# Optimization experiments

Hardware: AMD Instinct MI355X
Metric: run time of the kernel (lower is better)

Reference implementation:

```python
import jax, jax.numpy as jnp
import numpy as np

NEG_SLOPE = 0.2


def add_self_loops(edge_index, num_nodes):
    loop = jnp.arange(num_nodes, dtype=edge_index.dtype)
    return jnp.concatenate([edge_index, jnp.stack([loop, loop])], axis=1)


def gat_conv(x, edge_index, W, att_src, att_dst, bias, heads, out_ch, concat):
    # x: [N, F_in]; edge_index: [2, E]; W: [F_in, heads*out_ch]
    # att_src/att_dst: [heads, out_ch]; bias: [heads*out_ch] or [out_ch]
    N = x.shape[0]
    ei = add_self_loops(edge_index, N)
    src, dst = ei[0], ei[1]
    xw = (x @ W).reshape(N, heads, out_ch)          # [N, H, C]
    a_src = jnp.einsum('nhc,hc->nh', xw, att_src)    # [N, H]
    a_dst = jnp.einsum('nhc,hc->nh', xw, att_dst)    # [N, H]
    e = a_src[src] + a_dst[dst]                      # [E', H]
    e = jax.nn.leaky_relu(e, NEG_SLOPE)
    # segment softmax over edges grouped by destination node
    e_max = jax.ops.segment_max(e, dst, num_segments=N)  # [N, H]
    e_exp = jnp.exp(e - e_max[dst])
    denom = jax.ops.segment_sum(e_exp, dst, num_segments=N)  # [N, H]
    alpha = e_exp / denom[dst]                       # [E', H]
    msg = xw[src] * alpha[:, :, None]                # [E', H, C]
    out = jax.ops.segment_sum(msg, dst, num_segments=N)  # [N, H, C]
    if concat:
        out = out.reshape(N, heads * out_ch)
    else:
        out = out.mean(axis=1)
    return out + bias


def setup_inputs() -> dict:
    key = jax.random.key(0)
    ks = jax.random.split(key, 10)
    N, E = 100000, 1600000
    F_in, hid, heads, F_out = 128, 32, 4, 40
    s = 0.1
    x = jax.random.normal(ks[0], (N, F_in), dtype=jnp.float32)
    edge_index = jax.random.randint(ks[1], (2, E), 0, N, dtype=jnp.int64)
    W1 = jax.random.normal(ks[2], (F_in, heads * hid), dtype=jnp.float32) * s
    att_src1 = jax.random.normal(ks[3], (heads, hid), dtype=jnp.float32) * s
    att_dst1 = jax.random.normal(ks[4], (heads, hid), dtype=jnp.float32) * s
    b1 = jax.random.normal(ks[5], (heads * hid,), dtype=jnp.float32) * s
    W2 = jax.random.normal(ks[6], (heads * hid, F_out), dtype=jnp.float32) * s
    att_src2 = jax.random.normal(ks[7], (1, F_out), dtype=jnp.float32) * s
    att_dst2 = jax.random.normal(ks[8], (1, F_out), dtype=jnp.float32) * s
    b2 = jax.random.normal(ks[9], (F_out,), dtype=jnp.float32) * s
    return {"x": x, "edge_index": edge_index, "W1": W1, "att_src1": att_src1,
            "att_dst1": att_dst1, "b1": b1, "W2": W2, "att_src2": att_src2,
            "att_dst2": att_dst2, "b2": b2}


def reference(x, edge_index, W1, att_src1, att_dst1, b1, W2, att_src2, att_dst2, b2):
    h = gat_conv(x, edge_index, W1, att_src1, att_dst1, b1, heads=4, out_ch=32, concat=True)
    h = jax.nn.relu(h)
    out = gat_conv(h, edge_index, W2, att_src2, att_dst2, b2, heads=1, out_ch=40, concat=True)
    return out
```

## Files before the change

kernel.cpp:

```cpp
#include <hip/hip_runtime.h>
#include <hip/hip_bf16.h>

#define NEG_SLOPE 0.2f

typedef _Float16 f16;
typedef f16 f16x8 __attribute__((ext_vector_type(8)));
typedef float f32x4 __attribute__((ext_vector_type(4)));

__device__ __forceinline__ float lrelu(float v) { return v > 0.f ? v : NEG_SLOPE * v; }

__device__ __forceinline__ unsigned pack_h2(float a, float b) {
    union { f16 h[2]; unsigned u; } c;
    c.h[0] = (f16)a; c.h[1] = (f16)b;
    return c.u;
}
__device__ __forceinline__ float2 unpack_h2(unsigned u) {
    union { unsigned u; f16 h[2]; } c;
    c.u = u;
    return make_float2((float)c.h[0], (float)c.h[1]);
}

__global__ void k_detect(const int* __restrict__ ei32, int npairs, int* flag) {
    __shared__ int found;
    if (threadIdx.x == 0) found = 0;
    __syncthreads();
    for (int i = threadIdx.x; i < npairs; i += blockDim.x) {
        if (ei32[2 * i + 1] != 0) found = 1;
    }
    __syncthreads();
    if (threadIdx.x == 0) *flag = found ? 0 : 1;
}

__device__ __forceinline__ void load_edge(const void* ei, int f64, int e, int E, int& s, int& d) {
    if (f64) {
        const long long* p = (const long long*)ei;
        s = (int)p[e];
        d = (int)p[(long long)E + e];
    } else {
        const int* p = (const int*)ei;
        s = p[e];
        d = p[E + e];
    }
}

__global__ void k_degree(const void* __restrict__ ei, const int* __restrict__ flag,
                         int* __restrict__ deg, int* __restrict__ rank, int E) {
    int e = blockIdx.x * blockDim.x + threadIdx.x;
    if (e >= E) return;
    int s, d;
    load_edge(ei, *flag, e, E, s, d);
    rank[e] = atomicAdd(&deg[d], 1);
}

__global__ __launch_bounds__(1024) void k_scan_blk(const int* __restrict__ deg,
                                                   int* __restrict__ offsets,
                                                   int* __restrict__ blksum, int N) {
    __shared__ int wsums[16];
    const int t = threadIdx.x;
    const int lane = t & 63;
    const int wid = t >> 6;
    int idx = blockIdx.x * 4096 + t * 4;
    int v0 = (idx + 0 < N) ? deg[idx + 0] : 0;
    int v1 = (idx + 1 < N) ? deg[idx + 1] : 0;
    int v2 = (idx + 2 < N) ? deg[idx + 2] : 0;
    int v3 = (idx + 3 < N) ? deg[idx + 3] : 0;
    int s1 = v0 + v1, s2 = s1 + v2, s3 = s2 + v3;
    int inc = s3;
#pragma unroll
    for (int off = 1; off < 64; off <<= 1) {
        int y = __shfl_up(inc, off);
        if (lane >= off) inc += y;
    }
    if (lane == 63) wsums[wid] = inc;
    __syncthreads();
    if (wid == 0) {
        int v = (lane < 16) ? wsums[lane] : 0;
        int wi = v;
#pragma unroll
        for (int off = 1; off < 16; off <<= 1) {
            int y = __shfl_up(wi, off);
            if (lane >= off) wi += y;
        }
        if (lane < 16) wsums[lane] = wi - v;
        if (lane == 15) blksum[blockIdx.x] = wi;
    }
    __syncthreads();
    int excl = wsums[wid] + (inc - s3);
    if (idx + 0 < N) offsets[idx + 1] = excl + v0;
    if (idx + 1 < N) offsets[idx + 2] = excl + s1;
    if (idx + 2 < N) offsets[idx + 3] = excl + s2;
    if (idx + 3 < N) offsets[idx + 4] = excl + s3;
}

__global__ void k_scan_top(const int* __restrict__ blksum, int* __restrict__ blkoff, int G) {
    int l = threadIdx.x;
    int v = (l < G) ? blksum[l] : 0;
    int inc = v;
#pragma unroll
    for (int off = 1; off < 64; off <<= 1) {
        int y = __shfl_up(inc, off);
        if (l >= off) inc += y;
    }
    if (l < G) blkoff[l] = inc - v;
}

__global__ void k_scan_add(int* __restrict__ offsets, const int* __restrict__ blkoff, int N) {
    int n = blockIdx.x * blockDim.x + threadIdx.x;
    if (n >= N) return;
    offsets[n + 1] += blkoff[n >> 12];
    if (n == 0) offsets[0] = 0;
}

__global__ void k_scatter(const void* __restrict__ ei, const int* __restrict__ flag,
                          const int* __restrict__ offsets, const int* __restrict__ rank,
                          int* __restrict__ csr_src, int E) {
    int e = blockIdx.x * blockDim.x + threadIdx.x;
    if (e >= E) return;
    int s, d;
    load_edge(ei, *flag, e, E, s, d);
    csr_src[offsets[d] + rank[e]] = s;
}

__global__ void k_prep(const float* __restrict__ W1, const float* __restrict__ W2,
                       f16* __restrict__ W1t, f16* __restrict__ W2t) {
    int o = blockIdx.x * 256 + threadIdx.x;
    if (o < 128 * 128) {
        int n = o >> 7, k = o & 127;
        W1t[o] = (f16)W1[k * 128 + n];
    } else {
        int o2 = o - 128 * 128;
        if (o2 < 48 * 128) {
            int n = o2 >> 7, k = o2 & 127;
            W2t[o2] = (f16)(n < 40 ? W2[k * 40 + n] : 0.f);
        }
    }
}

__global__ __launch_bounds__(256) void k_gemm1(const float* __restrict__ X,
                                               const f16* __restrict__ W1t,
                                               f16* __restrict__ Af, int N) {
    __shared__ f16 sA[64 * 136];
    __shared__ f16 sB[128 * 136];
    const int t = threadIdx.x;
    const int row0 = blockIdx.x * 64;

    {
        int r = t >> 2, seg = t & 3;
        int row = row0 + r;
        if (row >= N) row = N - 1;
        const float4* xg = (const float4*)(X + (size_t)row * 128 + seg * 32);
        unsigned tmp[16];
#pragma unroll
        for (int j = 0; j < 8; j++) {
            float4 v = xg[j];
            tmp[2 * j]     = pack_h2(v.x, v.y);
            tmp[2 * j + 1] = pack_h2(v.z, v.w);
        }
        uint4* dst = (uint4*)&sA[r * 136 + seg * 32];
#pragma unroll
        for (int j = 0; j < 4; j++) dst[j] = ((uint4*)tmp)[j];
        int n = t >> 1, half = (t & 1) * 64;
        const uint4* src = (const uint4*)(W1t + n * 128 + half);
        uint4* dw = (uint4*)&sB[n * 136 + half];
#pragma unroll
        for (int j = 0; j < 8; j++) dw[j] = src[j];
    }
    __syncthreads();

    const int w = t >> 6, lane = t & 63, ln = lane & 15, q = lane >> 4;
    f32x4 acc[8];
#pragma unroll
    for (int c = 0; c < 8; c++) acc[c] = (f32x4){0.f, 0.f, 0.f, 0.f};

#pragma unroll
    for (int ks = 0; ks < 4; ks++) {
        f16x8 a = *(const f16x8*)&sA[(w * 16 + ln) * 136 + ks * 32 + q * 8];
#pragma unroll
        for (int c = 0; c < 8; c++) {
            f16x8 b = *(const f16x8*)&sB[(c * 16 + ln) * 136 + ks * 32 + q * 8];
            acc[c] = __builtin_amdgcn_mfma_f32_16x16x32_f16(a, b, acc[c], 0, 0, 0);
        }
    }

#pragma unroll
    for (int c = 0; c < 8; c++)
#pragma unroll
        for (int reg = 0; reg < 4; reg++) {
            int rg = row0 + w * 16 + q * 4 + reg;
            if (rg < N) Af[(size_t)rg * 128 + c * 16 + ln] = (f16)acc[c][reg];
        }
}

__global__ __launch_bounds__(256) void k_gemm2(const f16* __restrict__ Hf,
                                               const f16* __restrict__ W2t,
                                               f16* __restrict__ X2f, int N) {
    __shared__ f16 sA[64 * 136];
    __shared__ f16 sB[48 * 136];
    const int t = threadIdx.x;
    const int row0 = blockIdx.x * 64;
    {
        int r = t >> 2, seg = t & 3;
        int row = row0 + r;
        if (row >= N) row = N - 1;
        const uint4* hg = (const uint4*)(Hf + (size_t)row * 128 + seg * 32);
        uint4* dst = (uint4*)&sA[r * 136 + seg * 32];
#pragma unroll
        for (int j = 0; j < 4; j++) dst[j] = hg[j];
        const uint4* wsrc = (const uint4*)W2t;
#pragma unroll
        for (int u = t; u < 768; u += 256) {
            int o = u * 8;
            int n = o >> 7, ko = o & 127;
            *(uint4*)&sB[n * 136 + ko] = wsrc[u];
        }
    }
    __syncthreads();

    const int w = t >> 6, lane = t & 63, ln = lane & 15, q = lane >> 4;
    f32x4 acc[3];
#pragma unroll
    for (int c = 0; c < 3; c++) acc[c] = (f32x4){0.f, 0.f, 0.f, 0.f};

#pragma unroll
    for (int ks = 0; ks < 4; ks++) {
        f16x8 a = *(const f16x8*)&sA[(w * 16 + ln) * 136 + ks * 32 + q * 8];
#pragma unroll
        for (int c = 0; c < 3; c++) {
            f16x8 b = *(const f16x8*)&sB[(c * 16 + ln) * 136 + ks * 32 + q * 8];
            acc[c] = __builtin_amdgcn_mfma_f32_16x16x32_f16(a, b, acc[c], 0, 0, 0);
        }
    }

#pragma unroll
    for (int c = 0; c < 3; c++) {
        int col = c * 16 + ln;
        if (col < 40) {
#pragma unroll
            for (int reg = 0; reg < 4; reg++) {
                int rg = row0 + w * 16 + q * 4 + reg;
                if (rg < N) X2f[(size_t)rg * 40 + col] = (f16)acc[c][reg];
            }
        }
    }
}

__global__ void k_attn1(const f16* __restrict__ Af, const float* __restrict__ att_s,
                        const float* __restrict__ att_d, float* __restrict__ aS,
                        float* __restrict__ aD, int N) {
    int t = blockIdx.x * blockDim.x + threadIdx.x;
    if (t >= N * 4) return;
    int n = t >> 2, h = t & 3;
    const uint4* xr = (const uint4*)(Af + (size_t)n * 128 + h * 32);
    float ss = 0.f, sd = 0.f;
#pragma unroll
    for (int j = 0; j < 4; j++) {
        uint4 p = xr[j];
        float2 a0 = unpack_h2(p.x), a1 = unpack_h2(p.y), a2 = unpack_h2(p.z), a3 = unpack_h2(p.w);
        float xv[8] = {a0.x, a0.y, a1.x, a1.y, a2.x, a2.y, a3.x, a3.y};
        const float* as_ = att_s + h * 32 + j * 8;
        const float* ad_ = att_d + h * 32 + j * 8;
#pragma unroll
        for (int qq = 0; qq < 8; qq++) {
            ss += xv[qq] * as_[qq];
            sd += xv[qq] * ad_[qq];
        }
    }
    aS[t] = ss;
    aD[t] = sd;
}

__global__ void k_attn2(const f16* __restrict__ X2f, const float* __restrict__ att_s,
                        const float* __restrict__ att_d, float* __restrict__ aS,
                        float* __restrict__ aD, int N) {
    int n = blockIdx.x * blockDim.x + threadIdx.x;
    if (n >= N) return;
    const unsigned* xr = (const unsigned*)(X2f + (size_t)n * 40);
    float ss = 0.f, sd = 0.f;
#pragma unroll
    for (int j = 0; j < 20; j++) {
        float2 v = unpack_h2(xr[j]);
        ss += v.x * att_s[2 * j] + v.y * att_s[2 * j + 1];
        sd += v.x * att_d[2 * j] + v.y * att_d[2 * j + 1];
    }
    aS[n] = ss;
    aD[n] = sd;
}

__global__ __launch_bounds__(256) void k_alpha1(const int* __restrict__ offsets,
                                                const int* __restrict__ csr_src,
                                                const float* __restrict__ aS,
                                                const float* __restrict__ aD,
                                                float* __restrict__ alphaF,
                                                float* __restrict__ selfA, int N) {
    int n = blockIdx.x * 4 + (threadIdx.x >> 6);
    if (n >= N) return;
    int lane = threadIdx.x & 63;
    float4 aDn = *(const float4*)(aD + (size_t)n * 4);
    float4 aSn = *(const float4*)(aS + (size_t)n * 4);
    float r0 = 0.f, r1 = 0.f, r2 = 0.f, r3 = 0.f;
    int b = offsets[n], e = offsets[n + 1];
    for (int i = b + lane; i < e; i += 64) {
        int s = csr_src[i];
        float4 v = *(const float4*)(aS + (size_t)s * 4);
        r0 += __expf(lrelu(v.x + aDn.x));
        r1 += __expf(lrelu(v.y + aDn.y));
        r2 += __expf(lrelu(v.z + aDn.z));
        r3 += __expf(lrelu(v.w + aDn.w));
    }
#pragma unroll
    for (int m = 1; m < 64; m <<= 1) {
        r0 += __shfl_xor(r0, m);
        r1 += __shfl_xor(r1, m);
        r2 += __shfl_xor(r2, m);
        r3 += __shfl_xor(r3, m);
    }
    float w0 = __expf(lrelu(aSn.x + aDn.x));
    float w1 = __expf(lrelu(aSn.y + aDn.y));
    float w2 = __expf(lrelu(aSn.z + aDn.z));
    float w3 = __expf(lrelu(aSn.w + aDn.w));
    float i0 = 1.f / (r0 + w0), i1 = 1.f / (r1 + w1), i2 = 1.f / (r2 + w2), i3 = 1.f / (r3 + w3);
    if (lane == 0)
        *(float4*)(selfA + (size_t)n * 4) = make_float4(w0 * i0, w1 * i1, w2 * i2, w3 * i3);
    for (int i = b + lane; i < e; i += 64) {
        int s = csr_src[i];
        float4 v = *(const float4*)(aS + (size_t)s * 4);
        float4 al;
        al.x = __expf(lrelu(v.x + aDn.x)) * i0;
        al.y = __expf(lrelu(v.y + aDn.y)) * i1;
        al.z = __expf(lrelu(v.z + aDn.z)) * i2;
        al.w = __expf(lrelu(v.w + aDn.w)) * i3;
        *(float4*)(alphaF + (size_t)i * 4) = al;
    }
}

__global__ __launch_bounds__(256) void k_alpha2(const int* __restrict__ offsets,
                                                const int* __restrict__ csr_src,
                                                const float* __restrict__ aS,
                                                const float* __restrict__ aD,
                                                float* __restrict__ alpha,
                                                float* __restrict__ selfA, int N) {
    int n = blockIdx.x * 4 + (threadIdx.x >> 6);
    if (n >= N) return;
    int lane = threadIdx.x & 63;
    float aDn = aD[n];
    float r0 = 0.f;
    int b = offsets[n], e = offsets[n + 1];
    for (int i = b + lane; i < e; i += 64) {
        r0 += __expf(lrelu(aS[csr_src[i]] + aDn));
    }
#pragma unroll
    for (int m = 1; m < 64; m <<= 1) r0 += __shfl_xor(r0, m);
    float w0 = __expf(lrelu(aS[n] + aDn));
    float inv = 1.f / (r0 + w0);
    if (lane == 0) selfA[n] = w0 * inv;
    for (int i = b + lane; i < e; i += 64) {
        alpha[i] = __expf(lrelu(aS[csr_src[i]] + aDn)) * inv;
    }
}

__global__ __launch_bounds__(256) void k_msg1(const int* __restrict__ offsets,
                                              const int* __restrict__ csr_src,
                                              const float* __restrict__ alphaF,
                                              const float* __restrict__ selfA,
                                              const f16* __restrict__ Af,
                                              const float* __restrict__ b1,
                                              f16* __restrict__ Hf, int N) {
    int n = blockIdx.x * 4 + (threadIdx.x >> 6);
    if (n >= N) return;
    int lane = threadIdx.x & 63;
    int c0 = lane * 2;
    int h = lane >> 4;
    float sa = selfA[n * 4 + h];
    float2 pv = unpack_h2(*(const unsigned*)(Af + (size_t)n * 128 + c0));
    float acc0 = sa * pv.x, acc1 = sa * pv.y;
    int b = offsets[n], e = offsets[n + 1];
    int i = b;
    for (; i + 4 <= e; i += 4) {
        int s0 = csr_src[i], s1 = csr_src[i + 1], s2 = csr_src[i + 2], s3 = csr_src[i + 3];
        float a0 = alphaF[(size_t)i * 4 + h];
        float a1 = alphaF[(size_t)(i + 1) * 4 + h];
        float a2 = alphaF[(size_t)(i + 2) * 4 + h];
        float a3 = alphaF[(size_t)(i + 3) * 4 + h];
        unsigned r0 = *(const unsigned*)(Af + (size_t)s0 * 128 + c0);
        unsigned r1 = *(const unsigned*)(Af + (size_t)s1 * 128 + c0);
        unsigned r2 = *(const unsigned*)(Af + (size_t)s2 * 128 + c0);
        unsigned r3 = *(const unsigned*)(Af + (size_t)s3 * 128 + c0);
        float2 f0 = unpack_h2(r0), f1 = unpack_h2(r1), f2 = unpack_h2(r2), f3 = unpack_h2(r3);
        acc0 = fmaf(a0, f0.x, acc0); acc1 = fmaf(a0, f0.y, acc1);
        acc0 = fmaf(a1, f1.x, acc0); acc1 = fmaf(a1, f1.y, acc1);
        acc0 = fmaf(a2, f2.x, acc0); acc1 = fmaf(a2, f2.y, acc1);
        acc0 = fmaf(a3, f3.x, acc0); acc1 = fmaf(a3, f3.y, acc1);
    }
    for (; i < e; i++) {
        int s0 = csr_src[i];
        float a0 = alphaF[(size_t)i * 4 + h];
        float2 f0 = unpack_h2(*(const unsigned*)(Af + (size_t)s0 * 128 + c0));
        acc0 = fmaf(a0, f0.x, acc0); acc1 = fmaf(a0, f0.y, acc1);
    }
    float2 bb = *(const float2*)(b1 + c0);
    *(unsigned*)(Hf + (size_t)n * 128 + c0) =
        pack_h2(fmaxf(acc0 + bb.x, 0.f), fmaxf(acc1 + bb.y, 0.f));
}

__global__ __launch_bounds__(256) void k_msg2(const int* __restrict__ offsets,
                                              const int* __restrict__ csr_src,
                                              const float* __restrict__ alpha,
                                              const float* __restrict__ selfA,
                                              const f16* __restrict__ X2f,
                                              const float* __restrict__ b2,
                                              float* __restrict__ OUT, int N) {
    int wv = threadIdx.x >> 6, lane = threadIdx.x & 63;
    if (lane >= 60) return;
    int g = lane / 20;
    int li = lane - g * 20;
    int n = blockIdx.x * 12 + wv * 3 + g;
    if (n >= N) return;
    int c0 = li * 2;
    float sa = selfA[n];
    float2 pv = unpack_h2(*(const unsigned*)(X2f + (size_t)n * 40 + c0));
    float acc0 = sa * pv.x, acc1 = sa * pv.y;
    int b = offsets[n], e = offsets[n + 1];
    int i = b;
    for (; i + 4 <= e; i += 4) {
        int s0 = csr_src[i], s1 = csr_src[i + 1], s2 = csr_src[i + 2], s3 = csr_src[i + 3];
        float a0 = alpha[i], a1 = alpha[i + 1], a2 = alpha[i + 2], a3 = alpha[i + 3];
        float2 f0 = unpack_h2(*(const unsigned*)(X2f + (size_t)s0 * 40 + c0));
        float2 f1 = unpack_h2(*(const unsigned*)(X2f + (size_t)s1 * 40 + c0));
        float2 f2 = unpack_h2(*(const unsigned*)(X2f + (size_t)s2 * 40 + c0));
        float2 f3 = unpack_h2(*(const unsigned*)(X2f + (size_t)s3 * 40 + c0));
        acc0 += a0 * f0.x + a1 * f1.x + a2 * f2.x + a3 * f3.x;
        acc1 += a0 * f0.y + a1 * f1.y + a2 * f2.y + a3 * f3.y;
    }
    for (; i < e; i++) {
        int s0 = csr_src[i];
        float a0 = alpha[i];
        float2 f0 = unpack_h2(*(const unsigned*)(X2f + (size_t)s0 * 40 + c0));
        acc0 += a0 * f0.x;
        acc1 += a0 * f0.y;
    }
    float2 bb = *(const float2*)(b2 + c0);
    *(float2*)(OUT + (size_t)n * 40 + c0) = make_float2(acc0 + bb.x, acc1 + bb.y);
}

extern "C" void kernel_launch(void* const* d_in, const int* in_sizes, int n_in,
                              void* d_out, int out_size, void* d_ws, size_t ws_size,
                              hipStream_t stream) {
    const float* x   = (const float*)d_in[0];
    const void*  ei  = d_in[1];
    const float* W1  = (const float*)d_in[2];
    const float* as1 = (const float*)d_in[3];
    const float* ad1 = (const float*)d_in[4];
    const float* b1  = (const float*)d_in[5];
    const float* W2  = (const float*)d_in[6];
    const float* as2 = (const float*)d_in[7];
    const float* ad2 = (const float*)d_in[8];
    const float* b2  = (const float*)d_in[9];
    float* out = (float*)d_out;

    const int N = in_sizes[0] / 128;
    const int E = in_sizes[1] / 2;

    char* w = (char*)d_ws;
    auto alloc = [&](size_t bytes) {
        char* p = w;
        w += (bytes + 15) & ~(size_t)15;
        return p;
    };
    int* flag      = (int*)alloc(16);
    int* offsets   = (int*)alloc((size_t)(N + 1) * 4);
    int* deg       = (int*)alloc((size_t)N * 4);
    int* rank      = (int*)alloc((size_t)E * 4);
    int* csr_src   = (int*)alloc((size_t)E * 4);
    int* blksum    = (int*)alloc(64 * 4);
    int* blkoff    = (int*)alloc(64 * 4);
    float* aS1     = (float*)alloc((size_t)N * 4 * 4);
    float* aD1     = (float*)alloc((size_t)N * 4 * 4);
    float* aS2     = (float*)alloc((size_t)N * 4);
    float* aD2     = (float*)alloc((size_t)N * 4);
    float* alphaF  = (float*)alloc((size_t)E * 4 * 4);
    float* alpha2F = (float*)alloc((size_t)E * 4);
    float* selfA1  = (float*)alloc((size_t)N * 4 * 4);
    float* selfA2  = (float*)alloc((size_t)N * 4);
    f16* W1t       = (f16*)alloc(128 * 128 * 2);
    f16* W2t       = (f16*)alloc(48 * 128 * 2);
    f16* Af        = (f16*)alloc((size_t)N * 128 * 2);
    f16* X2f       = (f16*)alloc((size_t)N * 40 * 2);
    f16* Hf        = (f16*)alloc((size_t)N * 128 * 2);

    k_detect<<<1, 256, 0, stream>>>((const int*)ei, 1024, flag);
    k_prep<<<88, 256, 0, stream>>>(W1, W2, W1t, W2t);

    hipMemsetAsync(deg, 0, (size_t)N * 4, stream);
    k_degree<<<(E + 255) / 256, 256, 0, stream>>>(ei, flag, deg, rank, E);
    const int G = (N + 4095) / 4096;
    k_scan_blk<<<G, 1024, 0, stream>>>(deg, offsets, blksum, N);
    k_scan_top<<<1, 64, 0, stream>>>(blksum, blkoff, G);
    k_scan_add<<<(N + 255) / 256, 256, 0, stream>>>(offsets, blkoff, N);
    k_scatter<<<(E + 255) / 256, 256, 0, stream>>>(ei, flag, offsets, rank, csr_src, E);

    const int gb = (N + 63) / 64;
    k_gemm1<<<gb, 256, 0, stream>>>(x, W1t, Af, N);
    k_attn1<<<(N * 4 + 255) / 256, 256, 0, stream>>>(Af, as1, ad1, aS1, aD1, N);
    k_alpha1<<<(N + 3) / 4, 256, 0, stream>>>(offsets, csr_src, aS1, aD1, alphaF, selfA1, N);
    k_msg1<<<(N + 3) / 4, 256, 0, stream>>>(offsets, csr_src, alphaF, selfA1, Af, b1, Hf, N);

    k_gemm2<<<gb, 256, 0, stream>>>(Hf, W2t, X2f, N);
    k_attn2<<<(N + 255) / 256, 256, 0, stream>>>(X2f, as2, ad2, aS2, aD2, N);
    k_alpha2<<<(N + 3) / 4, 256, 0, stream>>>(offsets, csr_src, aS2, aD2, alpha2F, selfA2, N);
    k_msg2<<<(N + 11) / 12, 256, 0, stream>>>(offsets, csr_src, alpha2F, selfA2, X2f, b2, out, N);
}
```

Baseline: 448.8 us.

## Fuse softmax into message passing and split degree atomics per XCC

Removes the separate alpha kernels and computes unnormalized exp weights inline during aggregation, normalizing once at the end. This avoids writing and re-reading per-edge alpha arrays, at the cost of extra aS gathers and exps in the message kernels. Degree counting now uses per-XCC partial counters read from a hardware register, which cuts cross-die atomic contention. This adds a larger memset and an extra prefix kernel over the 8 partitions. Neither softmax form subtracts the segment max, so exp overflow remains possible as before.

```diff
diff --git a/kernel.cpp b/kernel.cpp
--- a/kernel.cpp
+++ b/kernel.cpp
@@ -2,6 +2,7 @@
 #include <hip/hip_bf16.h>
 
 #define NEG_SLOPE 0.2f
+#define HWREG_XCC_ID_FULL (((32 - 1) << 11) | (0 << 6) | 20)
 
 typedef _Float16 f16;
 typedef f16 f16x8 __attribute__((ext_vector_type(8)));
@@ -44,12 +45,27 @@
 }
 
 __global__ void k_degree(const void* __restrict__ ei, const int* __restrict__ flag,
-                         int* __restrict__ deg, int* __restrict__ rank, int E) {
+                         int* __restrict__ deg_part, int* __restrict__ rank, int N, int E) {
     int e = blockIdx.x * blockDim.x + threadIdx.x;
     if (e >= E) return;
     int s, d;
     load_edge(ei, *flag, e, E, s, d);
-    rank[e] = atomicAdd(&deg[d], 1);
+    int xcc = (int)(__builtin_amdgcn_s_getreg(HWREG_XCC_ID_FULL) & 7u);
+    int lr = atomicAdd(&deg_part[xcc * N + d], 1);
+    rank[e] = (xcc << 24) | lr;
+}
+
+__global__ void k_sumdeg(int* __restrict__ deg_part, int* __restrict__ deg, int N) {
+    int d = blockIdx.x * blockDim.x + threadIdx.x;
+    if (d >= N) return;
+    int p = 0;
+#pragma unroll
+    for (int x = 0; x < 8; x++) {
+        int t = deg_part[x * N + d];
+        deg_part[x * N + d] = p;
+        p += t;
+    }
+    deg[d] = p;
 }
 
 __global__ __launch_bounds__(1024) void k_scan_blk(const int* __restrict__ deg,
@@ -112,13 +128,17 @@
 }
 
 __global__ void k_scatter(const void* __restrict__ ei, const int* __restrict__ flag,
-                          const int* __restrict__ offsets, const int* __restrict__ rank,
-                          int* __restrict__ csr_src, int E) {
+                          const int* __restrict__ offsets, const int* __restrict__ deg_part,
+                          const int* __restrict__ rank, int* __restrict__ csr_src,
+                          int N, int E) {
     int e = blockIdx.x * blockDim.x + threadIdx.x;
     if (e >= E) return;
     int s, d;
     load_edge(ei, *flag, e, E, s, d);
-    csr_src[offsets[d] + rank[e]] = s;
+    int r = rank[e];
+    int xcc = r >> 24;
+    int lr = r & 0xFFFFFF;
+    csr_src[offsets[d] + deg_part[xcc * N + d] + lr] = s;
 }
 
 __global__ void k_prep(const float* __restrict__ W1, const float* __restrict__ W2,
@@ -286,82 +306,10 @@
     aD[n] = sd;
 }
 
-__global__ __launch_bounds__(256) void k_alpha1(const int* __restrict__ offsets,
-                                                const int* __restrict__ csr_src,
-                                                const float* __restrict__ aS,
-                                                const float* __restrict__ aD,
-                                                float* __restrict__ alphaF,
-                                                float* __restrict__ selfA, int N) {
-    int n = blockIdx.x * 4 + (threadIdx.x >> 6);
-    if (n >= N) return;
-    int lane = threadIdx.x & 63;
-    float4 aDn = *(const float4*)(aD + (size_t)n * 4);
-    float4 aSn = *(const float4*)(aS + (size_t)n * 4);
-    float r0 = 0.f, r1 = 0.f, r2 = 0.f, r3 = 0.f;
-    int b = offsets[n], e = offsets[n + 1];
-    for (int i = b + lane; i < e; i += 64) {
-        int s = csr_src[i];
-        float4 v = *(const float4*)(aS + (size_t)s * 4);
-        r0 += __expf(lrelu(v.x + aDn.x));
-        r1 += __expf(lrelu(v.y + aDn.y));
-        r2 += __expf(lrelu(v.z + aDn.z));
-        r3 += __expf(lrelu(v.w + aDn.w));
-    }
-#pragma unroll
-    for (int m = 1; m < 64; m <<= 1) {
-        r0 += __shfl_xor(r0, m);
-        r1 += __shfl_xor(r1, m);
-        r2 += __shfl_xor(r2, m);
-        r3 += __shfl_xor(r3, m);
-    }
-    float w0 = __expf(lrelu(aSn.x + aDn.x));
-    float w1 = __expf(lrelu(aSn.y + aDn.y));
-    float w2 = __expf(lrelu(aSn.z + aDn.z));
-    float w3 = __expf(lrelu(aSn.w + aDn.w));
-    float i0 = 1.f / (r0 + w0), i1 = 1.f / (r1 + w1), i2 = 1.f / (r2 + w2), i3 = 1.f / (r3 + w3);
-    if (lane == 0)
-        *(float4*)(selfA + (size_t)n * 4) = make_float4(w0 * i0, w1 * i1, w2 * i2, w3 * i3);
-    for (int i = b + lane; i < e; i += 64) {
-        int s = csr_src[i];
-        float4 v = *(const float4*)(aS + (size_t)s * 4);
-        float4 al;
-        al.x = __expf(lrelu(v.x + aDn.x)) * i0;
-        al.y = __expf(lrelu(v.y + aDn.y)) * i1;
-        al.z = __expf(lrelu(v.z + aDn.z)) * i2;
-        al.w = __expf(lrelu(v.w + aDn.w)) * i3;
-        *(float4*)(alphaF + (size_t)i * 4) = al;
-    }
-}
-
-__global__ __launch_bounds__(256) void k_alpha2(const int* __restrict__ offsets,
-                                                const int* __restrict__ csr_src,
-                                                const float* __restrict__ aS,
-                                                const float* __restrict__ aD,
-                                                float* __restrict__ alpha,
-                                                float* __restrict__ selfA, int N) {
-    int n = blockIdx.x * 4 + (threadIdx.x >> 6);
-    if (n >= N) return;
-    int lane = threadIdx.x & 63;
-    float aDn = aD[n];
-    float r0 = 0.f;
-    int b = offsets[n], e = offsets[n + 1];
-    for (int i = b + lane; i < e; i += 64) {
-        r0 += __expf(lrelu(aS[csr_src[i]] + aDn));
-    }
-#pragma unroll
-    for (int m = 1; m < 64; m <<= 1) r0 += __shfl_xor(r0, m);
-    float w0 = __expf(lrelu(aS[n] + aDn));
-    float inv = 1.f / (r0 + w0);
-    if (lane == 0) selfA[n] = w0 * inv;
-    for (int i = b + lane; i < e; i += 64) {
-        alpha[i] = __expf(lrelu(aS[csr_src[i]] + aDn)) * inv;
-    }
-}
-
 __global__ __launch_bounds__(256) void k_msg1(const int* __restrict__ offsets,
                                               const int* __restrict__ csr_src,
-                                              const float* __restrict__ alphaF,
-                                              const float* __restrict__ selfA,
+                                              const float* __restrict__ aS,
+                                              const float* __restrict__ aD,
                                               const f16* __restrict__ Af,
                                               const float* __restrict__ b1,
                                               f16* __restrict__ Hf, int N) {
@@ -370,42 +318,48 @@
     int lane = threadIdx.x & 63;
     int c0 = lane * 2;
     int h = lane >> 4;
-    float sa = selfA[n * 4 + h];
+    float adh = aD[n * 4 + h];
+    float wself = __expf(lrelu(aS[n * 4 + h] + adh));
     float2 pv = unpack_h2(*(const unsigned*)(Af + (size_t)n * 128 + c0));
-    float acc0 = sa * pv.x, acc1 = sa * pv.y;
+    float acc0 = wself * pv.x, acc1 = wself * pv.y;
+    float wsum = wself;
     int b = offsets[n], e = offsets[n + 1];
     int i = b;
     for (; i + 4 <= e; i += 4) {
         int s0 = csr_src[i], s1 = csr_src[i + 1], s2 = csr_src[i + 2], s3 = csr_src[i + 3];
-        float a0 = alphaF[(size_t)i * 4 + h];
-        float a1 = alphaF[(size_t)(i + 1) * 4 + h];
-        float a2 = alphaF[(size_t)(i + 2) * 4 + h];
-        float a3 = alphaF[(size_t)(i + 3) * 4 + h];
         unsigned r0 = *(const unsigned*)(Af + (size_t)s0 * 128 + c0);
         unsigned r1 = *(const unsigned*)(Af + (size_t)s1 * 128 + c0);
         unsigned r2 = *(const unsigned*)(Af + (size_t)s2 * 128 + c0);
         unsigned r3 = *(const unsigned*)(Af + (size_t)s3 * 128 + c0);
+        float w0 = __expf(lrelu(aS[s0 * 4 + h] + adh));
+        float w1 = __expf(lrelu(aS[s1 * 4 + h] + adh));
+        float w2 = __expf(lrelu(aS[s2 * 4 + h] + adh));
+        float w3 = __expf(lrelu(aS[s3 * 4 + h] + adh));
         float2 f0 = unpack_h2(r0), f1 = unpack_h2(r1), f2 = unpack_h2(r2), f3 = unpack_h2(r3);
-        acc0 = fmaf(a0, f0.x, acc0); acc1 = fmaf(a0, f0.y, acc1);
-        acc0 = fmaf(a1, f1.x, acc0); acc1 = fmaf(a1, f1.y, acc1);
-        acc0 = fmaf(a2, f2.x, acc0); acc1 = fmaf(a2, f2.y, acc1);
-        acc0 = fmaf(a3, f3.x, acc0); acc1 = fmaf(a3, f3.y, acc1);
+        acc0 = fmaf(w0, f0.x, acc0); acc1 = fmaf(w0, f0.y, acc1);
+        acc0 = fmaf(w1, f1.x, acc0); acc1 = fmaf(w1, f1.y, acc1);
+        acc0 = fmaf(w2, f2.x, acc0); acc1 = fmaf(w2, f2.y, acc1);
+        acc0 = fmaf(w3, f3.x, acc0); acc1 = fmaf(w3, f3.y, acc1);
+        wsum += (w0 + w1) + (w2 + w3);
     }
     for (; i < e; i++) {
         int s0 = csr_src[i];
-        float a0 = alphaF[(size_t)i * 4 + h];
-        float2 f0 = unpack_h2(*(const unsigned*)(Af + (size_t)s0 * 128 + c0));
-        acc0 = fmaf(a0, f0.x, acc0); acc1 = fmaf(a0, f0.y, acc1);
-    }
+        unsigned r0 = *(const unsigned*)(Af + (size_t)s0 * 128 + c0);
+        float w0 = __expf(lrelu(aS[s0 * 4 + h] + adh));
+        float2 f0 = unpack_h2(r0);
+        acc0 = fmaf(w0, f0.x, acc0); acc1 = fmaf(w0, f0.y, acc1);
+        wsum += w0;
+    }
+    float inv = 1.0f / wsum;
     float2 bb = *(const float2*)(b1 + c0);
     *(unsigned*)(Hf + (size_t)n * 128 + c0) =
-        pack_h2(fmaxf(acc0 + bb.x, 0.f), fmaxf(acc1 + bb.y, 0.f));
+        pack_h2(fmaxf(fmaf(acc0, inv, bb.x), 0.f), fmaxf(fmaf(acc1, inv, bb.y), 0.f));
 }
 
 __global__ __launch_bounds__(256) void k_msg2(const int* __restrict__ offsets,
                                               const int* __restrict__ csr_src,
-                                              const float* __restrict__ alpha,
-                                              const float* __restrict__ selfA,
+                                              const float* __restrict__ aS,
+                                              const float* __restrict__ aD,
                                               const f16* __restrict__ X2f,
                                               const float* __restrict__ b2,
                                               float* __restrict__ OUT, int N) {
@@ -416,30 +370,42 @@
     int n = blockIdx.x * 12 + wv * 3 + g;
     if (n >= N) return;
     int c0 = li * 2;
-    float sa = selfA[n];
+    float adh = aD[n];
+    float wself = __expf(lrelu(aS[n] + adh));
     float2 pv = unpack_h2(*(const unsigned*)(X2f + (size_t)n * 40 + c0));
-    float acc0 = sa * pv.x, acc1 = sa * pv.y;
+    float acc0 = wself * pv.x, acc1 = wself * pv.y;
+    float wsum = wself;
     int b = offsets[n], e = offsets[n + 1];
     int i = b;
     for (; i + 4 <= e; i += 4) {
         int s0 = csr_src[i], s1 = csr_src[i + 1], s2 = csr_src[i + 2], s3 = csr_src[i + 3];
-        float a0 = alpha[i], a1 = alpha[i + 1], a2 = alpha[i + 2], a3 = alpha[i + 3];
-        float2 f0 = unpack_h2(*(const unsigned*)(X2f + (size_t)s0 * 40 + c0));
-        float2 f1 = unpack_h2(*(const unsigned*)(X2f + (size_t)s1 * 40 + c0));
-        float2 f2 = unpack_h2(*(const unsigned*)(X2f + (size_t)s2 * 40 + c0));
-        float2 f3 = unpack_h2(*(const unsigned*)(X2f + (size_t)s3 * 40 + c0));
-        acc0 += a0 * f0.x + a1 * f1.x + a2 * f2.x + a3 * f3.x;
-        acc1 += a0 * f0.y + a1 * f1.y + a2 * f2.y + a3 * f3.y;
+        unsigned r0 = *(const unsigned*)(X2f + (size_t)s0 * 40 + c0);
+        unsigned r1 = *(const unsigned*)(X2f + (size_t)s1 * 40 + c0);
+        unsigned r2 = *(const unsigned*)(X2f + (size_t)s2 * 40 + c0);
+        unsigned r3 = *(const unsigned*)(X2f + (size_t)s3 * 40 + c0);
+        float w0 = __expf(lrelu(aS[s0] + adh));
+        float w1 = __expf(lrelu(aS[s1] + adh));
+        float w2 = __expf(lrelu(aS[s2] + adh));
+        float w3 = __expf(lrelu(aS[s3] + adh));
+        float2 f0 = unpack_h2(r0), f1 = unpack_h2(r1), f2 = unpack_h2(r2), f3 = unpack_h2(r3);
+        acc0 = fmaf(w0, f0.x, acc0); acc1 = fmaf(w0, f0.y, acc1);
+        acc0 = fmaf(w1, f1.x, acc0); acc1 = fmaf(w1, f1.y, acc1);
+        acc0 = fmaf(w2, f2.x, acc0); acc1 = fmaf(w2, f2.y, acc1);
+        acc0 = fmaf(w3, f3.x, acc0); acc1 = fmaf(w3, f3.y, acc1);
+        wsum += (w0 + w1) + (w2 + w3);
     }
     for (; i < e; i++) {
         int s0 = csr_src[i];
-        float a0 = alpha[i];
-        float2 f0 = unpack_h2(*(const unsigned*)(X2f + (size_t)s0 * 40 + c0));
-        acc0 += a0 * f0.x;
-        acc1 += a0 * f0.y;
-    }
+        unsigned r0 = *(const unsigned*)(X2f + (size_t)s0 * 40 + c0);
+        float w0 = __expf(lrelu(aS[s0] + adh));
+        float2 f0 = unpack_h2(r0);
+        acc0 = fmaf(w0, f0.x, acc0); acc1 = fmaf(w0, f0.y, acc1);
+        wsum += w0;
+    }
+    float inv = 1.0f / wsum;
     float2 bb = *(const float2*)(b2 + c0);
-    *(float2*)(OUT + (size_t)n * 40 + c0) = make_float2(acc0 + bb.x, acc1 + bb.y);
+    *(float2*)(OUT + (size_t)n * 40 + c0) =
+        make_float2(fmaf(acc0, inv, bb.x), fmaf(acc1, inv, bb.y));
 }
 
 extern "C" void kernel_launch(void* const* d_in, const int* in_sizes, int n_in,
@@ -469,6 +435,7 @@
     int* flag      = (int*)alloc(16);
     int* offsets   = (int*)alloc((size_t)(N + 1) * 4);
     int* deg       = (int*)alloc((size_t)N * 4);
+    int* deg_part  = (int*)alloc((size_t)N * 8 * 4);
     int* rank      = (int*)alloc((size_t)E * 4);
     int* csr_src   = (int*)alloc((size_t)E * 4);
     int* blksum    = (int*)alloc(64 * 4);
@@ -477,10 +444,6 @@
     float* aD1     = (float*)alloc((size_t)N * 4 * 4);
     float* aS2     = (float*)alloc((size_t)N * 4);
     float* aD2     = (float*)alloc((size_t)N * 4);
-    float* alphaF  = (float*)alloc((size_t)E * 4 * 4);
-    float* alpha2F = (float*)alloc((size_t)E * 4);
-    float* selfA1  = (float*)alloc((size_t)N * 4 * 4);
-    float* selfA2  = (float*)alloc((size_t)N * 4);
     f16* W1t       = (f16*)alloc(128 * 128 * 2);
     f16* W2t       = (f16*)alloc(48 * 128 * 2);
     f16* Af        = (f16*)alloc((size_t)N * 128 * 2);
@@ -490,22 +453,22 @@
     k_detect<<<1, 256, 0, stream>>>((const int*)ei, 1024, flag);
     k_prep<<<88, 256, 0, stream>>>(W1, W2, W1t, W2t);
 
-    hipMemsetAsync(deg, 0, (size_t)N * 4, stream);
-    k_degree<<<(E + 255) / 256, 256, 0, stream>>>(ei, flag, deg, rank, E);
+    hipMemsetAsync(deg_part, 0, (size_t)N * 8 * 4, stream);
+    k_degree<<<(E + 255) / 256, 256, 0, stream>>>(ei, flag, deg_part, rank, N, E);
+    k_sumdeg<<<(N + 255) / 256, 256, 0, stream>>>(deg_part, deg, N);
     const int G = (N + 4095) / 4096;
     k_scan_blk<<<G, 1024, 0, stream>>>(deg, offsets, blksum, N);
     k_scan_top<<<1, 64, 0, stream>>>(blksum, blkoff, G);
     k_scan_add<<<(N + 255) / 256, 256, 0, stream>>>(offsets, blkoff, N);
-    k_scatter<<<(E + 255) / 256, 256, 0, stream>>>(ei, flag, offsets, rank, csr_src, E);
+    k_scatter<<<(E + 255) / 256, 256, 0, stream>>>(ei, flag, offsets, deg_part, rank,
+                                                   csr_src, N, E);
 
     const int gb = (N + 63) / 64;
     k_gemm1<<<gb, 256, 0, stream>>>(x, W1t, Af, N);
     k_attn1<<<(N * 4 + 255) / 256, 256, 0, stream>>>(Af, as1, ad1, aS1, aD1, N);
-    k_alpha1<<<(N + 3) / 4, 256, 0, stream>>>(offsets, csr_src, aS1, aD1, alphaF, selfA1, N);
-    k_msg1<<<(N + 3) / 4, 256, 0, stream>>>(offsets, csr_src, alphaF, selfA1, Af, b1, Hf, N);
+    k_msg1<<<(N + 3) / 4, 256, 0, stream>>>(offsets, csr_src, aS1, aD1, Af, b1, Hf, N);
 
     k_gemm2<<<gb, 256, 0, stream>>>(Hf, W2t, X2f, N);
     k_attn2<<<(N + 255) / 256, 256, 0, stream>>>(X2f, as2, ad2, aS2, aD2, N);
-    k_alpha2<<<(N + 3) / 4, 256, 0, stream>>>(offsets, csr_src, aS2, aD2, alpha2F, selfA2, N);
-    k_msg2<<<(N + 11) / 12, 256, 0, stream>>>(offsets, csr_src, alpha2F, selfA2, X2f, b2, out, N);
-}
+    k_msg2<<<(N + 11) / 12, 256, 0, stream>>>(offsets, csr_src, aS2, aD2, X2f, b2, out, N);
+}
```

New measurement: 396.2 us. 11.7% less time.
